# Kernel optimization log

Hardware: AMD Instinct MI355X
Metric: run time of the kernel (lower is better)

## Reference

```python
import jax, jax.numpy as jnp
import numpy as np

N_NODES, N_EDGES, N_GRAPHS = 50000, 800000, 64
F_NODE, F_EDGE, F_GLOB, F_MSG, F_OUT, HID = 64, 64, 64, 64, 128, 32


def setup_inputs() -> dict:
    key = jax.random.key(0)
    ks = jax.random.split(key, 16)
    s = lambda fan_in: 1.0 / np.sqrt(fan_in)
    inp = {
        "x": jax.random.normal(ks[0], (N_NODES, F_NODE), dtype=jnp.float32),
        "edge_index": jax.random.randint(ks[1], (2, N_EDGES), 0, N_NODES),
        "edge_attr": jax.random.normal(ks[2], (N_EDGES, F_EDGE), dtype=jnp.float32),
        "u": jax.random.normal(ks[3], (N_GRAPHS, F_GLOB), dtype=jnp.float32),
        "batch": jnp.sort(jax.random.randint(ks[4], (N_NODES,), 0, N_GRAPHS)),
        # node_mlp_1: Lin(2*F_NODE+F_EDGE, 32) -> ReLU -> Lin(32, F_MSG) -> ReLU
        "W1": jax.random.normal(ks[5], (2 * F_NODE + F_EDGE, HID), dtype=jnp.float32) * s(2 * F_NODE + F_EDGE),
        "b1": jnp.zeros((HID,), jnp.float32),
        "W2": jax.random.normal(ks[6], (HID, F_MSG), dtype=jnp.float32) * s(HID),
        "b2": jnp.zeros((F_MSG,), jnp.float32),
        # node_mlp_2: Lin(2*F_MSG+F_NODE+F_GLOB, 32) -> ReLU -> Lin(32, F_OUT) -> ReLU
        "W3": jax.random.normal(ks[7], (2 * F_MSG + F_NODE + F_GLOB, HID), dtype=jnp.float32) * s(2 * F_MSG + F_NODE + F_GLOB),
        "b3": jnp.zeros((HID,), jnp.float32),
        "W4": jax.random.normal(ks[8], (HID, F_OUT), dtype=jnp.float32) * s(HID),
        "b4": jnp.zeros((F_OUT,), jnp.float32),
    }
    return inp


def reference(x, edge_index, edge_attr, u, batch, W1, b1, W2, b2, W3, b3, W4, b4):
    N = x.shape[0]
    row, col = edge_index[0], edge_index[1]
    # edge MLP (dropout off / eval mode)
    m = jnp.concatenate([x[row], x[col], edge_attr], axis=1)  # [E, 2F+Fe]
    m = jax.nn.relu(m @ W1 + b1)
    m = jax.nn.relu(m @ W2 + b2)  # [E, F_MSG]
    # scatter-mean and scatter-max onto destination nodes (col)
    cnt = jax.ops.segment_sum(jnp.ones((col.shape[0], 1), m.dtype), col, num_segments=N)  # [N,1]
    agg_mean = jax.ops.segment_sum(m, col, num_segments=N) / jnp.maximum(cnt, 1.0)
    agg_max = jax.ops.segment_max(m, col, num_segments=N)
    agg_max = jnp.where(cnt > 0, agg_max, 0.0)  # empty segments -> 0 (torch_scatter convention)
    # node MLP
    h = jnp.concatenate([x, agg_mean, agg_max, u[batch]], axis=1)
    h = jax.nn.relu(h @ W3 + b3)
    return jax.nn.relu(h @ W4 + b4)
```

## Files before the change

### kernel.cpp

```cpp
#include <hip/hip_runtime.h>
#include <hip/hip_bf16.h>
#include <stdint.h>

constexpr int FN   = 64;
constexpr int HIDN = 32;
constexpr int FMSG = 64;
constexpr int FOUT = 128;

using short8 = __attribute__((ext_vector_type(8))) short;
using f32x4  = __attribute__((ext_vector_type(4))) float;

union Frag { short8 v; uint32_t u[4]; };

__device__ __forceinline__ uint32_t packrn(float a, float b) {
    union { __hip_bfloat162 h; uint32_t u; } cv;
    cv.h = __float22bfloat162_rn(make_float2(a, b));
    return cv.u;
}
__device__ __forceinline__ float bf16_to_f(uint32_t h16) {
    return __uint_as_float(h16 << 16);
}

__device__ __forceinline__ int node_of(const int* __restrict__ offs, int N, int target) {
    int l = 0, r = N + 1;
    while (l + 1 < r) {
        const int m = (l + r) >> 1;
        if (offs[m] <= target) l = m; else r = m;
    }
    return l;
}

__global__ __launch_bounds__(256) void zero_cnt_kernel(int* __restrict__ cnt, int N)
{
    const int i = blockIdx.x * 256 + threadIdx.x;
    if (i < N) cnt[i] = 0;
}

__global__ __launch_bounds__(256) void hist_kernel(
    const int* __restrict__ ei, int* __restrict__ cnt, int* __restrict__ rank,
    int E)
{
    const int e = blockIdx.x * 256 + threadIdx.x;
    if (e < E) rank[e] = atomicAdd(cnt + ei[E + e], 1);
}

__global__ __launch_bounds__(128) void node_pre_kernel(
    const float* __restrict__ x,
    const float* __restrict__ W1, const float* __restrict__ b1,
    const float* __restrict__ W3, const float* __restrict__ b3,
    float* __restrict__ Pa, float* __restrict__ Pb, float* __restrict__ Qc,
    int N)
{
    __shared__ float xs_all[2 * 64 * 65];
    const int w    = threadIdx.x >> 6;
    const int lane = threadIdx.x & 63;
    float* xs = xs_all + w * (64 * 65);
    const int nbase = blockIdx.x * 128 + w * 64;
    if (nbase >= N) return;

#pragma unroll
    for (int j = 0; j < 16; ++j) {
        const int idx = j * 64 + lane;
        const int row = idx >> 4, cq = idx & 15;
        const int nr  = min(nbase + row, N - 1);
        const float4 v = *reinterpret_cast<const float4*>(x + (size_t)nr * FN + cq * 4);
        float* d = xs + row * 65 + cq * 4;
        d[0] = v.x; d[1] = v.y; d[2] = v.z; d[3] = v.w;
    }

    const int n = nbase + lane;
    if (n >= N) return;

    float a[HIDN], bq[HIDN], c[HIDN];
#pragma unroll
    for (int j = 0; j < HIDN; ++j) { a[j] = b1[j]; bq[j] = 0.0f; c[j] = b3[j]; }
    const float* xr = xs + lane * 65;
    const float* WA = W1;
    const float* WB = W1 + FN * HIDN;
    const float* WX = W3;
#pragma unroll 2
    for (int k = 0; k < FN; k += 4) {
        const float v0 = xr[k], v1 = xr[k + 1], v2 = xr[k + 2], v3 = xr[k + 3];
        const float* wa = WA + k * HIDN;
        const float* wb = WB + k * HIDN;
        const float* wc = WX + k * HIDN;
#pragma unroll
        for (int j = 0; j < HIDN; ++j) {
            float aj = a[j], bj = bq[j], cj = c[j];
            aj = fmaf(v0, wa[j], aj);            bj = fmaf(v0, wb[j], bj);            cj = fmaf(v0, wc[j], cj);
            aj = fmaf(v1, wa[HIDN + j], aj);     bj = fmaf(v1, wb[HIDN + j], bj);     cj = fmaf(v1, wc[HIDN + j], cj);
            aj = fmaf(v2, wa[2 * HIDN + j], aj); bj = fmaf(v2, wb[2 * HIDN + j], bj); cj = fmaf(v2, wc[2 * HIDN + j], cj);
            aj = fmaf(v3, wa[3 * HIDN + j], aj); bj = fmaf(v3, wb[3 * HIDN + j], bj); cj = fmaf(v3, wc[3 * HIDN + j], cj);
            a[j] = aj; bq[j] = bj; c[j] = cj;
        }
    }
    float4* pa = reinterpret_cast<float4*>(Pa + (size_t)n * HIDN);
    float4* pb = reinterpret_cast<float4*>(Pb + (size_t)n * HIDN);
    float4* qc = reinterpret_cast<float4*>(Qc + (size_t)n * HIDN);
#pragma unroll
    for (int q = 0; q < HIDN / 4; ++q) {
        pa[q] = make_float4(a[4*q], a[4*q+1], a[4*q+2], a[4*q+3]);
        pb[q] = make_float4(bq[4*q], bq[4*q+1], bq[4*q+2], bq[4*q+3]);
        qc[q] = make_float4(c[4*q], c[4*q+1], c[4*q+2], c[4*q+3]);
    }
}

__global__ __launch_bounds__(256) void prep_tail_kernel(
    const float* __restrict__ u,
    const float* __restrict__ W1, const float* __restrict__ W2,
    const float* __restrict__ W3, const float* __restrict__ W4,
    float* __restrict__ Qu,
    uint32_t* __restrict__ PW1, uint32_t* __restrict__ PW2,
    uint32_t* __restrict__ PW3, uint32_t* __restrict__ PW4,
    uint4* __restrict__ zbase, size_t zquads,
    int G, int BZ)
{
    const int b   = blockIdx.x;
    const int tid = threadIdx.x;

    if (b == 0) {
        const float* WC = W1 + 2 * FN * HIDN;
        for (int i = tid; i < 1024; i += 256) {
            const int j = i >> 5, k2 = i & 31;
            PW1[i] = packrn(WC[(2 * k2) * HIDN + j], WC[(2 * k2 + 1) * HIDN + j]);
        }
        for (int i = tid; i < 1024; i += 256) {
            const int j = i >> 4, k2 = i & 15;
            PW2[i] = packrn(W2[(2 * k2) * FMSG + j], W2[(2 * k2 + 1) * FMSG + j]);
        }
        const float* W3m = W3 + 64 * HIDN;
        for (int i = tid; i < 2048; i += 256) {
            const int j = i >> 6, k2 = i & 63;
            PW3[i] = packrn(W3m[(2 * k2) * HIDN + j], W3m[(2 * k2 + 1) * HIDN + j]);
        }
        for (int i = tid; i < 2048; i += 256) {
            const int j = i >> 4, k2 = i & 15;
            PW4[i] = packrn(W4[(2 * k2) * FOUT + j], W4[(2 * k2 + 1) * FOUT + j]);
        }
        const float* W3u = W3 + 192 * HIDN;
        for (int i = tid; i < G * HIDN; i += 256) {
            const int g = i >> 5, j = i & 31;
            const float* ur = u + (size_t)g * FN;
            float acc = 0.0f;
#pragma unroll 8
            for (int k = 0; k < FN; ++k) acc = fmaf(ur[k], W3u[k * HIDN + j], acc);
            Qu[i] = acc;
        }
        return;
    }
    const size_t stride = (size_t)BZ * 256;
    const uint4 z = make_uint4(0u, 0u, 0u, 0u);
    for (size_t i = (size_t)(b - 1) * 256 + tid; i < zquads; i += stride)
        zbase[i] = z;
}

__global__ __launch_bounds__(256) void scanA_kernel(
    const int* __restrict__ cnt, int* __restrict__ part, int N)
{
    __shared__ int red[256];
    const int tid  = threadIdx.x;
    const int base = blockIdx.x * 2048 + tid * 8;
    int s = 0;
    if (base + 8 <= N) {
        const int4 a = *reinterpret_cast<const int4*>(cnt + base);
        const int4 b = *reinterpret_cast<const int4*>(cnt + base + 4);
        s = a.x + a.y + a.z + a.w + b.x + b.y + b.z + b.w;
    } else {
        for (int i = base; i < min(base + 8, N); ++i) s += cnt[i];
    }
    red[tid] = s;
    __syncthreads();
    for (int d = 128; d > 0; d >>= 1) {
        if (tid < d) red[tid] += red[tid + d];
        __syncthreads();
    }
    if (tid == 0) part[blockIdx.x] = red[0];
}

__global__ __launch_bounds__(64) void scanB_kernel(
    const int* __restrict__ part, int* __restrict__ partx,
    int* __restrict__ offs, int NB, int N)
{
    if (threadIdx.x == 0) {
        int run = 0;
        for (int i = 0; i < NB; ++i) { partx[i] = run; run += part[i]; }
        offs[N] = run;
    }
}

__global__ __launch_bounds__(256) void scanC_kernel(
    const int* __restrict__ cnt, const int* __restrict__ partx,
    int* __restrict__ offs, int N)
{
    __shared__ int sb[256];
    const int tid  = threadIdx.x;
    const int base = blockIdx.x * 2048 + tid * 8;
    int v[8];
    int tsum = 0;
#pragma unroll
    for (int q = 0; q < 8; ++q) {
        const int i = base + q;
        v[q] = (i < N) ? cnt[i] : 0;
        tsum += v[q];
    }
    sb[tid] = tsum;
    __syncthreads();
    for (int d = 1; d < 256; d <<= 1) {
        const int t = (tid >= d) ? sb[tid - d] : 0;
        __syncthreads();
        sb[tid] += t;
        __syncthreads();
    }
    int run = partx[blockIdx.x] + sb[tid] - tsum;
#pragma unroll
    for (int q = 0; q < 8; ++q) {
        const int i = base + q;
        if (i < N) offs[i] = run;
        run += v[q];
    }
}

__global__ __launch_bounds__(256) void scatter_ntile_kernel(
    const int* __restrict__ ei, const int* __restrict__ offs,
    const int* __restrict__ rank, int4* __restrict__ re4,
    int2* __restrict__ ntile, int E, int N, int NT, int SB)
{
    const int tid = threadIdx.x;
    if ((int)blockIdx.x < SB) {
        const int e = blockIdx.x * 256 + tid;
        if (e >= E) return;
        const int row = ei[e];
        const int col = ei[E + e];
        const int pos = offs[col] + rank[e];
        re4[pos] = make_int4(row, col, e, 0);
    } else {
        const int t = ((int)blockIdx.x - SB) * 256 + tid;
        if (t >= NT) return;
        const int a = node_of(offs, N, t * 64);
        const int b = node_of(offs, N, min(t * 64 + 63, E - 1));
        ntile[t] = make_int2(a, b);
    }
}

__global__ __launch_bounds__(128) void fused_edge_mfma(
    const float* __restrict__ ea,
    const uint32_t* __restrict__ PW1, const uint32_t* __restrict__ PW2,
    const float* __restrict__ b2,
    const float* __restrict__ Pa, const float* __restrict__ Pb,
    const int4* __restrict__ re4, const int* __restrict__ offs,
    const int2* __restrict__ ntile,
    float* __restrict__ agg_sum, int* __restrict__ agg_maxb,
    int N, int E, int NT)
{
    __shared__ uint32_t smem_all[2 * 64 * 34];
    const int w    = threadIdx.x >> 6;
    const int t    = blockIdx.x * 2 + w;
    if (t >= NT) return;
    uint32_t* smem = smem_all + w * (64 * 34);
    const int lane = threadIdx.x & 63;
    const int l15  = lane & 15;
    const int l4   = lane >> 4;
    const int e0   = t * 64;
    const int e1   = min(e0 + 64, E);
    const int2 nrange = ntile[t];

    const int p = e0 + lane;
    const int4 rce = re4[min(p, E - 1)];
    {
        const float2* pa = reinterpret_cast<const float2*>(Pa + (size_t)rce.x * HIDN);
        const float2* pb = reinterpret_cast<const float2*>(Pb + (size_t)rce.y * HIDN);
        float2* dst = reinterpret_cast<float2*>(&smem[lane * 34]);
#pragma unroll
        for (int q = 0; q < 16; ++q) {
            const float2 a = pa[q], b = pb[q];
            dst[q] = make_float2(a.x + b.x, a.y + b.y);
        }
    }

    Frag B1[2][2];
#pragma unroll
    for (int nt = 0; nt < 2; ++nt)
#pragma unroll
        for (int ks = 0; ks < 2; ++ks) {
            const uint4 q = *reinterpret_cast<const uint4*>(
                &PW1[(nt * 16 + l15) * 32 + ks * 16 + l4 * 4]);
            B1[nt][ks].u[0] = q.x; B1[nt][ks].u[1] = q.y;
            B1[nt][ks].u[2] = q.z; B1[nt][ks].u[3] = q.w;
        }
    Frag B2f[4];
#pragma unroll
    for (int nt = 0; nt < 4; ++nt) {
        const uint4 q = *reinterpret_cast<const uint4*>(
            &PW2[(nt * 16 + l15) * 16 + l4 * 4]);
        B2f[nt].u[0] = q.x; B2f[nt].u[1] = q.y;
        B2f[nt].u[2] = q.z; B2f[nt].u[3] = q.w;
    }

    Frag A1[4][2];
#pragma unroll
    for (int mt = 0; mt < 4; ++mt) {
        const int eix = __shfl(rce.z, mt * 16 + l15, 64);
        const float* rp = ea + (size_t)eix * FN;
#pragma unroll
        for (int ks = 0; ks < 2; ++ks) {
            const float4* gp = reinterpret_cast<const float4*>(rp + ks * 32 + l4 * 8);
            const float4 f0 = gp[0], f1 = gp[1];
            A1[mt][ks].u[0] = packrn(f0.x, f0.y);
            A1[mt][ks].u[1] = packrn(f0.z, f0.w);
            A1[mt][ks].u[2] = packrn(f1.x, f1.y);
            A1[mt][ks].u[3] = packrn(f1.z, f1.w);
        }
    }

    f32x4 acc1[4][2];
    const float* Pl = reinterpret_cast<const float*>(smem);
#pragma unroll
    for (int mt = 0; mt < 4; ++mt)
#pragma unroll
        for (int nt = 0; nt < 2; ++nt)
#pragma unroll
            for (int r = 0; r < 4; ++r) {
                const int et = mt * 16 + l4 * 4 + r;
                acc1[mt][nt][r] = Pl[et * 34 + nt * 16 + l15];
            }
#pragma unroll
    for (int mt = 0; mt < 4; ++mt)
#pragma unroll
        for (int nt = 0; nt < 2; ++nt)
#pragma unroll
            for (int ks = 0; ks < 2; ++ks)
                acc1[mt][nt] = __builtin_amdgcn_mfma_f32_16x16x32_bf16(
                    A1[mt][ks].v, B1[nt][ks].v, acc1[mt][nt], 0, 0, 0);

    float* Hl = reinterpret_cast<float*>(smem);
#pragma unroll
    for (int mt = 0; mt < 4; ++mt)
#pragma unroll
        for (int nt = 0; nt < 2; ++nt)
#pragma unroll
            for (int r = 0; r < 4; ++r) {
                const int et = mt * 16 + l4 * 4 + r;
                Hl[et * 34 + nt * 16 + l15] = fmaxf(acc1[mt][nt][r], 0.0f);
            }

    Frag A2[4];
#pragma unroll
    for (int mt = 0; mt < 4; ++mt) {
        const float* hb = &Hl[(mt * 16 + l15) * 34 + l4 * 8];
        const float2 g0 = *reinterpret_cast<const float2*>(hb + 0);
        const float2 g1 = *reinterpret_cast<const float2*>(hb + 2);
        const float2 g2 = *reinterpret_cast<const float2*>(hb + 4);
        const float2 g3 = *reinterpret_cast<const float2*>(hb + 6);
        A2[mt].u[0] = packrn(g0.x, g0.y);
        A2[mt].u[1] = packrn(g1.x, g1.y);
        A2[mt].u[2] = packrn(g2.x, g2.y);
        A2[mt].u[3] = packrn(g3.x, g3.y);
    }

#pragma unroll
    for (int nt = 0; nt < 4; ++nt) {
        const float b2v = b2[nt * 16 + l15];
        f32x4 a2c[4];
#pragma unroll
        for (int mt = 0; mt < 4; ++mt) {
            a2c[mt] = (f32x4){0.f, 0.f, 0.f, 0.f};
            a2c[mt] = __builtin_amdgcn_mfma_f32_16x16x32_bf16(
                A2[mt].v, B2f[nt].v, a2c[mt], 0, 0, 0);
        }
        const int j = nt * 16 + l15;
#pragma unroll
        for (int mt = 0; mt < 4; ++mt)
#pragma unroll
            for (int rp2 = 0; rp2 < 2; ++rp2) {
                const int q2 = mt * 8 + l4 * 2 + rp2;
                const float v0 = fmaxf(a2c[mt][rp2 * 2]     + b2v, 0.0f);
                const float v1 = fmaxf(a2c[mt][rp2 * 2 + 1] + b2v, 0.0f);
                smem[q2 * 64 + (j ^ (((q2 >> 1) & 1) << 4))] = packrn(v0, v1);
            }
    }

    const int n0 = nrange.x, n1 = nrange.y;
    for (int n = n0; n <= n1; ++n) {
        const int s0 = offs[n], t0 = offs[n + 1];
        const int sl = max(s0, e0) - e0, tl = min(t0, e1) - e0;
        float sum = 0.0f, mx = 0.0f;
        int q = sl;
        if (q < tl && (q & 1)) {
            const int q2 = q >> 1;
            const uint32_t wv = smem[q2 * 64 + (lane ^ (((q2 >> 1) & 1) << 4))];
            const float v = bf16_to_f(wv >> 16);
            sum += v; mx = fmaxf(mx, v); ++q;
        }
        for (; q + 1 < tl; q += 2) {
            const int q2 = q >> 1;
            const uint32_t wv = smem[q2 * 64 + (lane ^ (((q2 >> 1) & 1) << 4))];
            const float v0 = bf16_to_f(wv & 0xffffu), v1 = bf16_to_f(wv >> 16);
            sum += v0 + v1; mx = fmaxf(mx, fmaxf(v0, v1));
        }
        if (q < tl) {
            const int q2 = q >> 1;
            const uint32_t wv = smem[q2 * 64 + (lane ^ (((q2 >> 1) & 1) << 4))];
            const float v = bf16_to_f(wv & 0xffffu);
            sum += v; mx = fmaxf(mx, v);
        }
        float* sp = agg_sum  + (size_t)n * FMSG + lane;
        int*   mp = agg_maxb + (size_t)n * FMSG + lane;
        if (s0 >= e0 && t0 <= e1) {
            *sp = sum;
            *mp = __float_as_int(mx);
        } else {
            unsafeAtomicAdd(sp, sum);
            atomicMax(mp, __float_as_int(mx));
        }
    }
}

__global__ __launch_bounds__(256) void node_mfma(
    const float* __restrict__ Qc, const float* __restrict__ Qu,
    const int*   __restrict__ batch,
    const uint32_t* __restrict__ PW3, const uint32_t* __restrict__ PW4,
    const float* __restrict__ b4,
    const float* __restrict__ agg_sum, const int* __restrict__ agg_maxb,
    const int*   __restrict__ offs,
    float* __restrict__ out, int N)
{
    __shared__ float Hl_all[4 * 32 * 34];
    const int w    = threadIdx.x >> 6;
    float* Hl      = Hl_all + w * (32 * 34);
    const int lane = threadIdx.x & 63;
    const int l15  = lane & 15;
    const int l4   = lane >> 4;
    const int n0   = blockIdx.x * 128 + w * 32;
    if (n0 >= N) return;

    f32x4 acc1[2][2];
#pragma unroll
    for (int mt = 0; mt < 2; ++mt)
#pragma unroll
        for (int r = 0; r < 4; ++r) {
            const int nc = min(n0 + mt * 16 + l4 * 4 + r, N - 1);
            const int g  = batch[nc];
#pragma unroll
            for (int nt = 0; nt < 2; ++nt)
                acc1[mt][nt][r] = Qc[(size_t)nc * HIDN + nt * 16 + l15]
                                + Qu[(size_t)g  * HIDN + nt * 16 + l15];
        }

    int   arn[2];
    float ainv[2];
#pragma unroll
    for (int mt = 0; mt < 2; ++mt) {
        arn[mt] = min(n0 + mt * 16 + l15, N - 1);
        const int deg = offs[arn[mt] + 1] - offs[arn[mt]];
        ainv[mt] = (deg > 0) ? 1.0f / (float)deg : 0.0f;
    }

    Frag B3[2][4];
#pragma unroll
    for (int nt = 0; nt < 2; ++nt)
#pragma unroll
        for (int ks = 0; ks < 4; ++ks) {
            const uint4 q = *reinterpret_cast<const uint4*>(
                &PW3[(nt * 16 + l15) * 64 + ks * 16 + l4 * 4]);
            B3[nt][ks].u[0] = q.x; B3[nt][ks].u[1] = q.y;
            B3[nt][ks].u[2] = q.z; B3[nt][ks].u[3] = q.w;
        }

#pragma unroll
    for (int ks = 0; ks < 4; ++ks) {
        Frag A[2];
        if (ks < 2) {
#pragma unroll
            for (int mt = 0; mt < 2; ++mt) {
                const float4* gp = reinterpret_cast<const float4*>(
                    agg_sum + (size_t)arn[mt] * FMSG + ks * 32 + l4 * 8);
                const float4 f0 = gp[0], f1 = gp[1];
                const float s = ainv[mt];
                A[mt].u[0] = packrn(f0.x * s, f0.y * s);
                A[mt].u[1] = packrn(f0.z * s, f0.w * s);
                A[mt].u[2] = packrn(f1.x * s, f1.y * s);
                A[mt].u[3] = packrn(f1.z * s, f1.w * s);
            }
        } else {
#pragma unroll
            for (int mt = 0; mt < 2; ++mt) {
                const uint4* gp = reinterpret_cast<const uint4*>(
                    agg_maxb + (size_t)arn[mt] * FMSG + (ks - 2) * 32 + l4 * 8);
                const uint4 u0 = gp[0], u1 = gp[1];
                A[mt].u[0] = packrn(__uint_as_float(u0.x), __uint_as_float(u0.y));
                A[mt].u[1] = packrn(__uint_as_float(u0.z), __uint_as_float(u0.w));
                A[mt].u[2] = packrn(__uint_as_float(u1.x), __uint_as_float(u1.y));
                A[mt].u[3] = packrn(__uint_as_float(u1.z), __uint_as_float(u1.w));
            }
        }
#pragma unroll
        for (int mt = 0; mt < 2; ++mt)
#pragma unroll
            for (int nt = 0; nt < 2; ++nt)
                acc1[mt][nt] = __builtin_amdgcn_mfma_f32_16x16x32_bf16(
                    A[mt].v, B3[nt][ks].v, acc1[mt][nt], 0, 0, 0);
    }

#pragma unroll
    for (int mt = 0; mt < 2; ++mt)
#pragma unroll
        for (int nt = 0; nt < 2; ++nt)
#pragma unroll
            for (int r = 0; r < 4; ++r) {
                const int rw = mt * 16 + l4 * 4 + r;
                Hl[rw * 34 + nt * 16 + l15] = fmaxf(acc1[mt][nt][r], 0.0f);
            }

    Frag A2[2];
#pragma unroll
    for (int mt = 0; mt < 2; ++mt) {
        const float* hb = &Hl[(mt * 16 + l15) * 34 + l4 * 8];
        const float2 g0 = *reinterpret_cast<const float2*>(hb + 0);
        const float2 g1 = *reinterpret_cast<const float2*>(hb + 2);
        const float2 g2 = *reinterpret_cast<const float2*>(hb + 4);
        const float2 g3 = *reinterpret_cast<const float2*>(hb + 6);
        A2[mt].u[0] = packrn(g0.x, g0.y);
        A2[mt].u[1] = packrn(g1.x, g1.y);
        A2[mt].u[2] = packrn(g2.x, g2.y);
        A2[mt].u[3] = packrn(g3.x, g3.y);
    }

#pragma unroll
    for (int nt = 0; nt < 8; ++nt) {
        Frag B4f;
        const uint4 q = *reinterpret_cast<const uint4*>(
            &PW4[(nt * 16 + l15) * 16 + l4 * 4]);
        B4f.u[0] = q.x; B4f.u[1] = q.y; B4f.u[2] = q.z; B4f.u[3] = q.w;
        const float b4v = b4[nt * 16 + l15];
        f32x4 tacc[2];
#pragma unroll
        for (int mt = 0; mt < 2; ++mt) {
            tacc[mt] = (f32x4){0.f, 0.f, 0.f, 0.f};
            tacc[mt] = __builtin_amdgcn_mfma_f32_16x16x32_bf16(
                A2[mt].v, B4f.v, tacc[mt], 0, 0, 0);
        }
#pragma unroll
        for (int mt = 0; mt < 2; ++mt)
#pragma unroll
            for (int r = 0; r < 4; ++r) {
                const int node = n0 + mt * 16 + l4 * 4 + r;
                if (node < N)
                    out[(size_t)node * FOUT + nt * 16 + l15] =
                        fmaxf(tacc[mt][r] + b4v, 0.0f);
            }
    }
}

extern "C" void kernel_launch(void* const* d_in, const int* in_sizes, int n_in,
                              void* d_out, int out_size, void* d_ws, size_t ws_size,
                              hipStream_t stream)
{
    const float* x     = (const float*)d_in[0];
    const int*   ei    = (const int*)  d_in[1];
    const float* ea    = (const float*)d_in[2];
    const float* u     = (const float*)d_in[3];
    const int*   batch = (const int*)  d_in[4];
    const float* W1    = (const float*)d_in[5];
    const float* b1    = (const float*)d_in[6];
    const float* W2    = (const float*)d_in[7];
    const float* b2    = (const float*)d_in[8];
    const float* W3    = (const float*)d_in[9];
    const float* b3    = (const float*)d_in[10];
    const float* W4    = (const float*)d_in[11];
    const float* b4    = (const float*)d_in[12];
    float* out = (float*)d_out;

    const int N = in_sizes[0] / FN;
    const int E = in_sizes[1] / 2;
    const int G = in_sizes[3] / FN;
    const int NT = (E + 63) / 64;

    char* wp = (char*)d_ws;
    auto take = [&](size_t bytes) -> void* {
        void* r = (void*)wp;
        wp += (bytes + 255) & ~(size_t)255;
        return r;
    };
    float*    agg_sum  = (float*)   take((size_t)N * FMSG * 4);
    int*      agg_maxb = (int*)     take((size_t)N * FMSG * 4);
    char*     zero_end = wp;
    int*      cnt      = (int*)     take((size_t)N * 4);
    int*      offs     = (int*)     take(((size_t)N + 1) * 4);
    int*      rank     = (int*)     take((size_t)E * 4);
    int4*     re4      = (int4*)    take((size_t)E * 16);
    int2*     ntile    = (int2*)    take((size_t)NT * 8);
    float*    Pa       = (float*)   take((size_t)N * HIDN * 4);
    float*    Pb       = (float*)   take((size_t)N * HIDN * 4);
    float*    Qc       = (float*)   take((size_t)N * HIDN * 4);
    float*    Qu       = (float*)   take((size_t)G * HIDN * 4);
    uint32_t* PW1      = (uint32_t*)take(1024 * 4);
    uint32_t* PW2      = (uint32_t*)take(1024 * 4);
    uint32_t* PW3      = (uint32_t*)take(2048 * 4);
    uint32_t* PW4      = (uint32_t*)take(2048 * 4);
    int*      part     = (int*)     take(64 * 4);
    int*      partx    = (int*)     take(64 * 4);

    const int BZ = 256;
    const int NB = (N + 2047) / 2048;
    const int SB = (E + 255) / 256;
    const int TB = (NT + 255) / 256;
    const size_t zquads = (size_t)(zero_end - (char*)agg_sum) / 16;

    zero_cnt_kernel<<<(N + 255) / 256, 256, 0, stream>>>(cnt, N);
    hist_kernel    <<<(E + 255) / 256, 256, 0, stream>>>(ei, cnt, rank, E);
    node_pre_kernel<<<(N + 127) / 128, 128, 0, stream>>>(
        x, W1, b1, W3, b3, Pa, Pb, Qc, N);
    prep_tail_kernel<<<1 + BZ, 256, 0, stream>>>(
        u, W1, W2, W3, W4, Qu, PW1, PW2, PW3, PW4,
        (uint4*)agg_sum, zquads, G, BZ);
    scanA_kernel   <<<NB, 256, 0, stream>>>(cnt, part, N);
    scanB_kernel   <<<1, 64, 0, stream>>>(part, partx, offs, NB, N);
    scanC_kernel   <<<NB, 256, 0, stream>>>(cnt, partx, offs, N);
    scatter_ntile_kernel<<<SB + TB, 256, 0, stream>>>(
        ei, offs, rank, re4, ntile, E, N, NT, SB);
    fused_edge_mfma<<<(NT + 1) / 2, 128, 0, stream>>>(
        ea, PW1, PW2, b2, Pa, Pb, re4, offs, ntile, agg_sum, agg_maxb, N, E, NT);
    node_mfma      <<<(N + 127) / 128, 256, 0, stream>>>(
        Qc, Qu, batch, PW3, PW4, b4, agg_sum, agg_maxb, offs, out, N);
}
```

Measured before the change: 246.1 us.

## Merge histogram, node precompute and weight prep into one launch; drop scanB

Combines hist_kernel, node_pre_kernel and prep_tail_kernel into a single mega_prep_kernel whose block ranges pick the role, so independent work shares one launch. The histogram now does 8 edges per thread with vectorized index loads. The node precompute uses 256-thread blocks and stages x in two 32-column halves to shrink shared memory. scanB is removed: each scanC block sums the preceding partials itself and offs[N] is set to E. The aim is fewer kernel launches and serial single-thread steps, at the cost of heterogeneous blocks contending within one grid.

```diff
diff --git a/kernel.cpp b/kernel.cpp
--- a/kernel.cpp
+++ b/kernel.cpp
@@ -36,89 +36,101 @@
     if (i < N) cnt[i] = 0;
 }
 
-__global__ __launch_bounds__(256) void hist_kernel(
+__global__ __launch_bounds__(256) void mega_prep_kernel(
     const int* __restrict__ ei, int* __restrict__ cnt, int* __restrict__ rank,
-    int E)
-{
-    const int e = blockIdx.x * 256 + threadIdx.x;
-    if (e < E) rank[e] = atomicAdd(cnt + ei[E + e], 1);
-}
-
-__global__ __launch_bounds__(128) void node_pre_kernel(
-    const float* __restrict__ x,
+    const float* __restrict__ x, const float* __restrict__ u,
     const float* __restrict__ W1, const float* __restrict__ b1,
+    const float* __restrict__ W2,
     const float* __restrict__ W3, const float* __restrict__ b3,
+    const float* __restrict__ W4,
     float* __restrict__ Pa, float* __restrict__ Pb, float* __restrict__ Qc,
-    int N)
-{
-    __shared__ float xs_all[2 * 64 * 65];
-    const int w    = threadIdx.x >> 6;
-    const int lane = threadIdx.x & 63;
-    float* xs = xs_all + w * (64 * 65);
-    const int nbase = blockIdx.x * 128 + w * 64;
-    if (nbase >= N) return;
-
-#pragma unroll
-    for (int j = 0; j < 16; ++j) {
-        const int idx = j * 64 + lane;
-        const int row = idx >> 4, cq = idx & 15;
-        const int nr  = min(nbase + row, N - 1);
-        const float4 v = *reinterpret_cast<const float4*>(x + (size_t)nr * FN + cq * 4);
-        float* d = xs + row * 65 + cq * 4;
-        d[0] = v.x; d[1] = v.y; d[2] = v.z; d[3] = v.w;
-    }
-
-    const int n = nbase + lane;
-    if (n >= N) return;
-
-    float a[HIDN], bq[HIDN], c[HIDN];
-#pragma unroll
-    for (int j = 0; j < HIDN; ++j) { a[j] = b1[j]; bq[j] = 0.0f; c[j] = b3[j]; }
-    const float* xr = xs + lane * 65;
-    const float* WA = W1;
-    const float* WB = W1 + FN * HIDN;
-    const float* WX = W3;
-#pragma unroll 2
-    for (int k = 0; k < FN; k += 4) {
-        const float v0 = xr[k], v1 = xr[k + 1], v2 = xr[k + 2], v3 = xr[k + 3];
-        const float* wa = WA + k * HIDN;
-        const float* wb = WB + k * HIDN;
-        const float* wc = WX + k * HIDN;
-#pragma unroll
-        for (int j = 0; j < HIDN; ++j) {
-            float aj = a[j], bj = bq[j], cj = c[j];
-            aj = fmaf(v0, wa[j], aj);            bj = fmaf(v0, wb[j], bj);            cj = fmaf(v0, wc[j], cj);
-            aj = fmaf(v1, wa[HIDN + j], aj);     bj = fmaf(v1, wb[HIDN + j], bj);     cj = fmaf(v1, wc[HIDN + j], cj);
-            aj = fmaf(v2, wa[2 * HIDN + j], aj); bj = fmaf(v2, wb[2 * HIDN + j], bj); cj = fmaf(v2, wc[2 * HIDN + j], cj);
-            aj = fmaf(v3, wa[3 * HIDN + j], aj); bj = fmaf(v3, wb[3 * HIDN + j], bj); cj = fmaf(v3, wc[3 * HIDN + j], cj);
-            a[j] = aj; bq[j] = bj; c[j] = cj;
-        }
-    }
-    float4* pa = reinterpret_cast<float4*>(Pa + (size_t)n * HIDN);
-    float4* pb = reinterpret_cast<float4*>(Pb + (size_t)n * HIDN);
-    float4* qc = reinterpret_cast<float4*>(Qc + (size_t)n * HIDN);
-#pragma unroll
-    for (int q = 0; q < HIDN / 4; ++q) {
-        pa[q] = make_float4(a[4*q], a[4*q+1], a[4*q+2], a[4*q+3]);
-        pb[q] = make_float4(bq[4*q], bq[4*q+1], bq[4*q+2], bq[4*q+3]);
-        qc[q] = make_float4(c[4*q], c[4*q+1], c[4*q+2], c[4*q+3]);
-    }
-}
-
-__global__ __launch_bounds__(256) void prep_tail_kernel(
-    const float* __restrict__ u,
-    const float* __restrict__ W1, const float* __restrict__ W2,
-    const float* __restrict__ W3, const float* __restrict__ W4,
     float* __restrict__ Qu,
     uint32_t* __restrict__ PW1, uint32_t* __restrict__ PW2,
     uint32_t* __restrict__ PW3, uint32_t* __restrict__ PW4,
     uint4* __restrict__ zbase, size_t zquads,
-    int G, int BZ)
-{
+    int E, int N, int G, int BH, int BPN, int BZ)
+{
+    __shared__ float xs_all[4 * 64 * 33];
     const int b   = blockIdx.x;
     const int tid = threadIdx.x;
 
-    if (b == 0) {
+    if (b < BH) {
+        const int base = (b * 256 + tid) * 8;
+        if (base + 8 <= E) {
+            const int4 c0 = *reinterpret_cast<const int4*>(ei + E + base);
+            const int4 c1 = *reinterpret_cast<const int4*>(ei + E + base + 4);
+            int4 r0, r1;
+            r0.x = atomicAdd(cnt + c0.x, 1);
+            r0.y = atomicAdd(cnt + c0.y, 1);
+            r0.z = atomicAdd(cnt + c0.z, 1);
+            r0.w = atomicAdd(cnt + c0.w, 1);
+            r1.x = atomicAdd(cnt + c1.x, 1);
+            r1.y = atomicAdd(cnt + c1.y, 1);
+            r1.z = atomicAdd(cnt + c1.z, 1);
+            r1.w = atomicAdd(cnt + c1.w, 1);
+            *reinterpret_cast<int4*>(rank + base)     = r0;
+            *reinterpret_cast<int4*>(rank + base + 4) = r1;
+        } else {
+            for (int e = base; e < E; ++e) rank[e] = atomicAdd(cnt + ei[E + e], 1);
+        }
+        return;
+    }
+    if (b < BH + BPN) {
+        const int w    = tid >> 6;
+        const int lane = tid & 63;
+        float* xs = xs_all + w * (64 * 33);
+        const int nbase = (b - BH) * 256 + w * 64;
+        if (nbase >= N) return;
+
+        float a[HIDN], bq[HIDN], cc[HIDN];
+#pragma unroll
+        for (int j = 0; j < HIDN; ++j) { a[j] = b1[j]; bq[j] = 0.0f; cc[j] = b3[j]; }
+
+#pragma unroll
+        for (int c = 0; c < 2; ++c) {
+#pragma unroll
+            for (int i = 0; i < 8; ++i) {
+                const int idx = i * 64 + lane;
+                const int row = idx >> 3, cq = idx & 7;
+                const int nr  = min(nbase + row, N - 1);
+                const float4 v = *reinterpret_cast<const float4*>(
+                    x + (size_t)nr * FN + c * 32 + cq * 4);
+                float* d = xs + row * 33 + cq * 4;
+                d[0] = v.x; d[1] = v.y; d[2] = v.z; d[3] = v.w;
+            }
+            const float* xr = xs + lane * 33;
+#pragma unroll 2
+            for (int k = 0; k < 32; k += 4) {
+                const float v0 = xr[k], v1 = xr[k + 1], v2 = xr[k + 2], v3 = xr[k + 3];
+                const int kg = c * 32 + k;
+                const float* wa = W1 + kg * HIDN;
+                const float* wb = W1 + FN * HIDN + kg * HIDN;
+                const float* wc = W3 + kg * HIDN;
+#pragma unroll
+                for (int j = 0; j < HIDN; ++j) {
+                    float aj = a[j], bj = bq[j], cj = cc[j];
+                    aj = fmaf(v0, wa[j], aj);            bj = fmaf(v0, wb[j], bj);            cj = fmaf(v0, wc[j], cj);
+                    aj = fmaf(v1, wa[HIDN + j], aj);     bj = fmaf(v1, wb[HIDN + j], bj);     cj = fmaf(v1, wc[HIDN + j], cj);
+                    aj = fmaf(v2, wa[2 * HIDN + j], aj); bj = fmaf(v2, wb[2 * HIDN + j], bj); cj = fmaf(v2, wc[2 * HIDN + j], cj);
+                    aj = fmaf(v3, wa[3 * HIDN + j], aj); bj = fmaf(v3, wb[3 * HIDN + j], bj); cj = fmaf(v3, wc[3 * HIDN + j], cj);
+                    a[j] = aj; bq[j] = bj; cc[j] = cj;
+                }
+            }
+        }
+        const int n = nbase + lane;
+        if (n >= N) return;
+        float4* pa = reinterpret_cast<float4*>(Pa + (size_t)n * HIDN);
+        float4* pb = reinterpret_cast<float4*>(Pb + (size_t)n * HIDN);
+        float4* qc = reinterpret_cast<float4*>(Qc + (size_t)n * HIDN);
+#pragma unroll
+        for (int q = 0; q < HIDN / 4; ++q) {
+            pa[q] = make_float4(a[4*q], a[4*q+1], a[4*q+2], a[4*q+3]);
+            pb[q] = make_float4(bq[4*q], bq[4*q+1], bq[4*q+2], bq[4*q+3]);
+            qc[q] = make_float4(cc[4*q], cc[4*q+1], cc[4*q+2], cc[4*q+3]);
+        }
+        return;
+    }
+    if (b == BH + BPN) {
         const float* WC = W1 + 2 * FN * HIDN;
         for (int i = tid; i < 1024; i += 256) {
             const int j = i >> 5, k2 = i & 31;
@@ -150,7 +162,7 @@
     }
     const size_t stride = (size_t)BZ * 256;
     const uint4 z = make_uint4(0u, 0u, 0u, 0u);
-    for (size_t i = (size_t)(b - 1) * 256 + tid; i < zquads; i += stride)
+    for (size_t i = (size_t)(b - BH - BPN - 1) * 256 + tid; i < zquads; i += stride)
         zbase[i] = z;
 }
 
@@ -177,23 +189,15 @@
     if (tid == 0) part[blockIdx.x] = red[0];
 }
 
-__global__ __launch_bounds__(64) void scanB_kernel(
-    const int* __restrict__ part, int* __restrict__ partx,
-    int* __restrict__ offs, int NB, int N)
-{
-    if (threadIdx.x == 0) {
-        int run = 0;
-        for (int i = 0; i < NB; ++i) { partx[i] = run; run += part[i]; }
-        offs[N] = run;
-    }
-}
-
 __global__ __launch_bounds__(256) void scanC_kernel(
-    const int* __restrict__ cnt, const int* __restrict__ partx,
-    int* __restrict__ offs, int N)
+    const int* __restrict__ cnt, const int* __restrict__ part,
+    int* __restrict__ offs, int NB, int N, int E)
 {
     __shared__ int sb[256];
     const int tid  = threadIdx.x;
+    int px = 0;
+    for (int i = 0; i < (int)blockIdx.x; ++i) px += part[i];
+
     const int base = blockIdx.x * 2048 + tid * 8;
     int v[8];
     int tsum = 0;
@@ -211,13 +215,14 @@
         sb[tid] += t;
         __syncthreads();
     }
-    int run = partx[blockIdx.x] + sb[tid] - tsum;
+    int run = px + sb[tid] - tsum;
 #pragma unroll
     for (int q = 0; q < 8; ++q) {
         const int i = base + q;
         if (i < N) offs[i] = run;
         run += v[q];
     }
+    if (blockIdx.x == 0 && tid == 0) offs[N] = E;
 }
 
 __global__ __launch_bounds__(256) void scatter_ntile_kernel(
@@ -598,24 +603,22 @@
     uint32_t* PW3      = (uint32_t*)take(2048 * 4);
     uint32_t* PW4      = (uint32_t*)take(2048 * 4);
     int*      part     = (int*)     take(64 * 4);
-    int*      partx    = (int*)     take(64 * 4);
-
-    const int BZ = 256;
-    const int NB = (N + 2047) / 2048;
-    const int SB = (E + 255) / 256;
-    const int TB = (NT + 255) / 256;
+
+    const int BH  = (E + 2047) / 2048;
+    const int BPN = (N + 255) / 256;
+    const int BZ  = 256;
+    const int NB  = (N + 2047) / 2048;
+    const int SB  = (E + 255) / 256;
+    const int TB  = (NT + 255) / 256;
     const size_t zquads = (size_t)(zero_end - (char*)agg_sum) / 16;
 
     zero_cnt_kernel<<<(N + 255) / 256, 256, 0, stream>>>(cnt, N);
-    hist_kernel    <<<(E + 255) / 256, 256, 0, stream>>>(ei, cnt, rank, E);
-    node_pre_kernel<<<(N + 127) / 128, 128, 0, stream>>>(
-        x, W1, b1, W3, b3, Pa, Pb, Qc, N);
-    prep_tail_kernel<<<1 + BZ, 256, 0, stream>>>(
-        u, W1, W2, W3, W4, Qu, PW1, PW2, PW3, PW4,
-        (uint4*)agg_sum, zquads, G, BZ);
+    mega_prep_kernel<<<BH + BPN + 1 + BZ, 256, 0, stream>>>(
+        ei, cnt, rank, x, u, W1, b1, W2, W3, b3, W4,
+        Pa, Pb, Qc, Qu, PW1, PW2, PW3, PW4,
+        (uint4*)agg_sum, zquads, E, N, G, BH, BPN, BZ);
     scanA_kernel   <<<NB, 256, 0, stream>>>(cnt, part, N);
-    scanB_kernel   <<<1, 64, 0, stream>>>(part, partx, offs, NB, N);
-    scanC_kernel   <<<NB, 256, 0, stream>>>(cnt, partx, offs, N);
+    scanC_kernel   <<<NB, 256, 0, stream>>>(cnt, part, offs, NB, N, E);
     scatter_ntile_kernel<<<SB + TB, 256, 0, stream>>>(
         ei, offs, rank, re4, ntile, E, N, NT, SB);
     fused_edge_mfma<<<(NT + 1) / 2, 128, 0, stream>>>(
```

Result: faster. 198.4 us (-19.4%).
